# Kernel optimization log

Measured on AMD Instinct MI355X. Metric: run time of the kernel, lower is better.

## Reference

```python
import jax, jax.numpy as jnp
import numpy as np

DIM = 384
DIM_HEAD = 32
HEADS = DIM // DIM_HEAD  # 12
WIN = 8
DIM_FF = 1536
FUSED = DIM + DIM + DIM_FF  # 2304


def setup_inputs() -> dict:
    key = jax.random.key(0)
    ks = jax.random.split(key, 8)
    B, H, W = 16, 64, 64
    x = jax.random.normal(ks[0], (B, DIM, H, W), dtype=jnp.float32)
    s = lambda fan_in: 1.0 / np.sqrt(fan_in)
    w_fused = jax.random.normal(ks[1], (FUSED, DIM), dtype=jnp.float32) * s(DIM)
    w_gate = jax.random.normal(ks[2], (HEADS, DIM), dtype=jnp.float32) * s(DIM)
    b_gate = jnp.full((HEADS,), 0.5, dtype=jnp.float32)  # init_constant_(0.5)
    w_attn_out = jax.random.normal(ks[3], (DIM, DIM), dtype=jnp.float32) * s(DIM)
    w_ff_out = jax.random.normal(ks[4], (DIM, DIM_FF), dtype=jnp.float32) * s(DIM_FF)
    # StarReLU learnable scalars (metaformer defaults)
    sr_scale = jnp.asarray(0.8944, dtype=jnp.float32)
    sr_bias = jnp.asarray(-0.4472, dtype=jnp.float32)
    return {"x": x, "w_fused": w_fused, "w_gate": w_gate, "b_gate": b_gate,
            "w_attn_out": w_attn_out, "w_ff_out": w_ff_out,
            "sr_scale": sr_scale, "sr_bias": sr_bias}


def reference(x, w_fused, w_gate, b_gate, w_attn_out, w_ff_out, sr_scale, sr_bias):
    B, C, H, W = x.shape
    p = WIN
    gh, gw = H // p, W // p
    n = p * p
    # b c (h p1) (w p2) -> (b h w) (p1 p2) c
    xw = x.reshape(B, C, gh, p, gw, p).transpose(0, 2, 4, 3, 5, 1).reshape(B * gh * gw, n, C)
    fused = jnp.einsum('bnc,fc->bnf', xw, w_fused)  # [Bw, n, 2304]
    q, kv, x_ff = jnp.split(fused, [DIM, 2 * DIM], axis=-1)
    # b n (h d) -> b h n d
    q = q.reshape(-1, n, HEADS, DIM_HEAD).transpose(0, 2, 1, 3)
    kv = kv.reshape(-1, n, HEADS, DIM_HEAD).transpose(0, 2, 1, 3)
    scale = 1.0 / np.sqrt(DIM_HEAD)
    scores = jnp.einsum('bhnd,bhmd->bhnm', q, kv) * scale
    attn = jax.nn.softmax(scores, axis=-1)
    x_attn = jnp.einsum('bhnm,bhmd->bhnd', attn, kv)  # kv is both key and value
    gate = jnp.einsum('bnc,hc->bnh', xw, w_gate) + b_gate  # [Bw, n, heads]
    x_attn = x_attn * jax.nn.sigmoid(gate.transpose(0, 2, 1)[..., None])
    x_attn = x_attn.transpose(0, 2, 1, 3).reshape(-1, n, DIM)
    ff = sr_scale * jnp.square(jax.nn.relu(x_ff)) + sr_bias  # StarReLU
    out = jnp.einsum('bnc,oc->bno', x_attn, w_attn_out) + jnp.einsum('bnf,of->bno', ff, w_ff_out)
    # (b h w) (p1 p2) c -> b c (h p1) (w p2)
    out = out.reshape(B, gh, gw, p, p, C).transpose(0, 5, 1, 3, 2, 4).reshape(B, C, H, W)
    return out
```

## Files before the change

### kernel.cpp

```cpp
#include <hip/hip_runtime.h>
#include <hip/hip_bf16.h>

typedef __bf16 bf16x8 __attribute__((ext_vector_type(8), may_alias));
typedef float f32x4 __attribute__((ext_vector_type(4), may_alias));
typedef unsigned short ushort_a __attribute__((may_alias));

#define MFMA(a, b, c) __builtin_amdgcn_mfma_f32_16x16x32_bf16(a, b, c, 0, 0, 0)

__device__ __forceinline__ unsigned short f2bf(float f) {
  return __builtin_bit_cast(unsigned short, (__bf16)f);
}


__global__ __launch_bounds__(256) void prep_weights(
    const float* __restrict__ wf, const float* __restrict__ wg,
    const float* __restrict__ wao, const float* __restrict__ wfo,
    unsigned short* __restrict__ ws) {
  int i = blockIdx.x * 256 + threadIdx.x;
  if (i < 884736) { ws[i] = f2bf(wf[i]); return; }
  int j = i - 884736;
  if (j < 6144) { ws[i] = f2bf(j < 4608 ? wg[j] : 0.0f); return; }
  j -= 6144;
  if (j < 147456) { ws[i] = f2bf(wao[j]); return; }
  j -= 147456;
  if (j < 589824) ws[i] = f2bf(wfo[j]);
}


__global__ __launch_bounds__(512, 2) void fused_main(
    const float* __restrict__ x,
    const float* __restrict__ bgate,
    const float* __restrict__ srs,
    const float* __restrict__ srb,
    const unsigned short* __restrict__ wsb,
    float* __restrict__ out) {
  const unsigned short* wfB  = wsb;
  const unsigned short* wgB  = wsb + 884736;
  const unsigned short* waoB = wsb + 890880;
  const unsigned short* wfoB = wsb + 1038336;

  __shared__ __align__(16) char smem[114688];
  char* As  = smem;
  char* Stg = smem + 98304;

  const int tid = threadIdx.x;
  const int lane = tid & 63, wave = tid >> 6;
  const int l15 = lane & 15, l4 = lane >> 4;
  const int pair = wave >> 1, nb = (wave & 1) * 32;
  char* PB  = smem + 49152 + pair * 12288;
  char* KTb = PB + 8192;

  const int g  = blockIdx.x;
  const int wi = (g & 7) * 128 + (g >> 3);
  const int b = wi >> 6, ghi = (wi >> 3) & 7, gwi = wi & 7;
  const int h0 = ghi * 8, w0 = gwi * 8;

  {
    const float* xb = x + (size_t)b * 1572864 + h0 * 64 + w0;
    for (int it = 0; it < 6; ++it) {
      int idx = it * 512 + tid;
      int c = idx % 384, p1 = idx / 384;
      const float* src = xb + (size_t)c * 4096 + p1 * 64;
      float4 v0 = *(const float4*)src;
      float4 v1 = *(const float4*)(src + 4);
      float f[8] = {v0.x, v0.y, v0.z, v0.w, v1.x, v1.y, v1.z, v1.w};
#pragma unroll
      for (int jj = 0; jj < 8; ++jj) {
        int row = p1 * 8 + jj;
        int byte = (row * 768 + c * 2) ^ ((row & 7) << 4);
        *(ushort_a*)(As + byte) = f2bf(f[jj]);
      }
    }
  }
  const float ss = srs[0], sbi = srb[0];
  __syncthreads();

  auto ldA = [&](int row, int ks) -> bf16x8 {
    int byte = (row * 768 + ks * 64 + l4 * 16) ^ ((row & 7) << 4);
    return *(const bf16x8*)(As + byte);
  };

  f32x4 gfr[2] = {};
  {
    const unsigned short* wg0 = wgB + (size_t)l15 * 384 + l4 * 8;
#pragma unroll 2
    for (int ks = 0; ks < 12; ++ks) {
      bf16x8 bg = *(const bf16x8*)(wg0 + ks * 32);
      bf16x8 a0 = ldA(nb + l15, ks), a1 = ldA(nb + 16 + l15, ks);
      gfr[0] = MFMA(a0, bg, gfr[0]);
      gfr[1] = MFMA(a1, bg, gfr[1]);
    }
    float gb = (l15 < 12) ? bgate[l15] : 0.0f;
    gfr[0] += gb;
    gfr[1] += gb;
  }

  f32x4 of[4][3] = {};

#pragma unroll 1
  for (int r = 0; r < 3; ++r) {
    const int h = r * 4 + pair;
    f32x4 qf[2][2] = {}, kf[2][2] = {};
    const unsigned short* wq = wfB + ((size_t)(h * 32) + l15) * 384 + l4 * 8;
    const unsigned short* wk = wq + (size_t)384 * 384;
#pragma unroll 2
    for (int ks = 0; ks < 12; ++ks) {
      bf16x8 a0 = ldA(nb + l15, ks), a1 = ldA(nb + 16 + l15, ks);
#pragma unroll
      for (int nt = 0; nt < 2; ++nt) {
        bf16x8 bq = *(const bf16x8*)(wq + (size_t)nt * 16 * 384 + ks * 32);
        bf16x8 bk = *(const bf16x8*)(wk + (size_t)nt * 16 * 384 + ks * 32);
        qf[0][nt] = MFMA(a0, bq, qf[0][nt]);
        qf[1][nt] = MFMA(a1, bq, qf[1][nt]);
        kf[0][nt] = MFMA(a0, bk, kf[0][nt]);
        kf[1][nt] = MFMA(a1, bk, kf[1][nt]);
      }
    }
#pragma unroll
    for (int mt = 0; mt < 2; ++mt)
#pragma unroll
      for (int nt = 0; nt < 2; ++nt)
#pragma unroll
        for (int rr = 0; rr < 4; ++rr) {
          int n = nb + mt * 16 + l4 * 4 + rr;
          int d = nt * 16 + l15;
          int sw = (n & 7) << 4;
          *(ushort_a*)(PB + ((n * 128 + d * 2) ^ sw)) =
              f2bf(qf[mt][nt][rr] * 0.176776695f);
          unsigned short kvv = f2bf(kf[mt][nt][rr]);
          *(ushort_a*)(PB + ((n * 128 + 64 + d * 2) ^ sw)) = kvv;
          *(ushort_a*)(KTb + ((d * 128 + n * 2) ^ ((d & 7) << 4))) = kvv;
        }
    __syncthreads();
    f32x4 sf[2][4] = {};
    {
      bf16x8 bkv[4];
#pragma unroll
      for (int ni = 0; ni < 4; ++ni) {
        int m = ni * 16 + l15;
        bkv[ni] = *(const bf16x8*)(PB + ((m * 128 + 64 + l4 * 16) ^ ((m & 7) << 4)));
      }
#pragma unroll
      for (int mt = 0; mt < 2; ++mt) {
        int n = nb + mt * 16 + l15;
        bf16x8 aq = *(const bf16x8*)(PB + ((n * 128 + l4 * 16) ^ ((n & 7) << 4)));
#pragma unroll
        for (int ni = 0; ni < 4; ++ni) sf[mt][ni] = MFMA(aq, bkv[ni], sf[mt][ni]);
      }
    }
    __syncthreads();
#pragma unroll
    for (int mt = 0; mt < 2; ++mt) {
#pragma unroll
      for (int rr = 0; rr < 4; ++rr) {
        float v0 = sf[mt][0][rr], v1 = sf[mt][1][rr],
              v2 = sf[mt][2][rr], v3 = sf[mt][3][rr];
        float mx = fmaxf(fmaxf(v0, v1), fmaxf(v2, v3));
        mx = fmaxf(mx, __shfl_xor(mx, 1, 64));
        mx = fmaxf(mx, __shfl_xor(mx, 2, 64));
        mx = fmaxf(mx, __shfl_xor(mx, 4, 64));
        mx = fmaxf(mx, __shfl_xor(mx, 8, 64));
        float e0 = __expf(v0 - mx), e1 = __expf(v1 - mx),
              e2 = __expf(v2 - mx), e3 = __expf(v3 - mx);
        float sm = e0 + e1 + e2 + e3;
        sm += __shfl_xor(sm, 1, 64);
        sm += __shfl_xor(sm, 2, 64);
        sm += __shfl_xor(sm, 4, 64);
        sm += __shfl_xor(sm, 8, 64);
        float rs = 1.0f / sm;
        int n = nb + mt * 16 + l4 * 4 + rr;
        int base = n * 128, sw = (n & 7) << 4;
        *(ushort_a*)(PB + ((base + l15 * 2) ^ sw))      = f2bf(e0 * rs);
        *(ushort_a*)(PB + ((base + 32 + l15 * 2) ^ sw)) = f2bf(e1 * rs);
        *(ushort_a*)(PB + ((base + 64 + l15 * 2) ^ sw)) = f2bf(e2 * rs);
        *(ushort_a*)(PB + ((base + 96 + l15 * 2) ^ sw)) = f2bf(e3 * rs);
      }
    }
    f32x4 xo[2][2] = {};
#pragma unroll
    for (int ks = 0; ks < 2; ++ks) {
      bf16x8 bv[2];
#pragma unroll
      for (int nt = 0; nt < 2; ++nt) {
        int d = nt * 16 + l15;
        bv[nt] = *(const bf16x8*)(KTb + ((d * 128 + ks * 64 + l4 * 16) ^ ((d & 7) << 4)));
      }
#pragma unroll
      for (int mt = 0; mt < 2; ++mt) {
        int n = nb + mt * 16 + l15;
        bf16x8 ap = *(const bf16x8*)(PB + ((n * 128 + ks * 64 + l4 * 16) ^ ((n & 7) << 4)));
        xo[mt][0] = MFMA(ap, bv[0], xo[mt][0]);
        xo[mt][1] = MFMA(ap, bv[1], xo[mt][1]);
      }
    }
#pragma unroll
    for (int mt = 0; mt < 2; ++mt) {
#pragma unroll
      for (int rr = 0; rr < 4; ++rr) {
        float gv = __shfl(gfr[mt][rr], (lane & 48) | h, 64);
        float sg = 1.0f / (1.0f + __expf(-gv));
        int n = nb + mt * 16 + l4 * 4 + rr;
        int sw = (n & 7) << 4;
        int c0 = pair * 32 + l15;
        *(ushort_a*)(Stg + ((n * 256 + c0 * 2) ^ sw))        = f2bf(xo[mt][0][rr] * sg);
        *(ushort_a*)(Stg + ((n * 256 + (c0 + 16) * 2) ^ sw)) = f2bf(xo[mt][1][rr] * sg);
      }
    }
    __syncthreads();
    {
      const unsigned short* wao0 =
          waoB + (size_t)(wave * 48 + l15) * 384 + r * 128 + l4 * 8;
#pragma unroll
      for (int ks = 0; ks < 4; ++ks) {
        int kb = ks * 64 + l4 * 16, sz = (l15 & 7) << 4;
        bf16x8 a0 = *(const bf16x8*)(Stg + ((l15 * 256 + kb) ^ sz));
        bf16x8 a1 = *(const bf16x8*)(Stg + (((16 + l15) * 256 + kb) ^ sz));
        bf16x8 a2 = *(const bf16x8*)(Stg + (((32 + l15) * 256 + kb) ^ sz));
        bf16x8 a3 = *(const bf16x8*)(Stg + (((48 + l15) * 256 + kb) ^ sz));
#pragma unroll
        for (int nt = 0; nt < 3; ++nt) {
          bf16x8 bw = *(const bf16x8*)(wao0 + (size_t)nt * 16 * 384 + ks * 32);
          of[0][nt] = MFMA(a0, bw, of[0][nt]);
          of[1][nt] = MFMA(a1, bw, of[1][nt]);
          of[2][nt] = MFMA(a2, bw, of[2][nt]);
          of[3][nt] = MFMA(a3, bw, of[3][nt]);
        }
      }
    }
  }

#pragma unroll 1
  for (int tg = 0; tg < 6; ++tg) {
    f32x4 ffr[4][2] = {};
    const unsigned short* wfin0 =
        wfB + (size_t)(768 + tg * 256 + wave * 16 + l15) * 384 + l4 * 8;
    const unsigned short* wfin1 = wfin0 + (size_t)128 * 384;
#pragma unroll 2
    for (int ks = 0; ks < 12; ++ks) {
      bf16x8 a0 = ldA(l15, ks), a1 = ldA(16 + l15, ks),
             a2 = ldA(32 + l15, ks), a3 = ldA(48 + l15, ks);
      bf16x8 bw0 = *(const bf16x8*)(wfin0 + ks * 32);
      ffr[0][0] = MFMA(a0, bw0, ffr[0][0]);
      ffr[1][0] = MFMA(a1, bw0, ffr[1][0]);
      ffr[2][0] = MFMA(a2, bw0, ffr[2][0]);
      ffr[3][0] = MFMA(a3, bw0, ffr[3][0]);
      bf16x8 bw1 = *(const bf16x8*)(wfin1 + ks * 32);
      ffr[0][1] = MFMA(a0, bw1, ffr[0][1]);
      ffr[1][1] = MFMA(a1, bw1, ffr[1][1]);
      ffr[2][1] = MFMA(a2, bw1, ffr[2][1]);
      ffr[3][1] = MFMA(a3, bw1, ffr[3][1]);
    }
#pragma unroll
    for (int u = 0; u < 2; ++u) {
      char* fb = smem + 49152 + u * 16384;
#pragma unroll
      for (int mt = 0; mt < 4; ++mt)
#pragma unroll
        for (int rr = 0; rr < 4; ++rr) {
          float v = fmaxf(ffr[mt][u][rr], 0.0f);
          v = ss * v * v + sbi;
          int n = mt * 16 + l4 * 4 + rr;
          int cw = wave * 16 + l15;
          *(ushort_a*)(fb + ((n * 256 + cw * 2) ^ ((n & 7) << 4))) = f2bf(v);
        }
    }
    __syncthreads();
#pragma unroll 1
    for (int u = 0; u < 2; ++u) {
      char* fb = smem + 49152 + u * 16384;
      const unsigned short* wfo2 =
          wfoB + (size_t)(wave * 48 + l15) * 1536 + (tg * 2 + u) * 128 + l4 * 8;
#pragma unroll
      for (int ks = 0; ks < 4; ++ks) {
        int kb = ks * 64 + l4 * 16, sz = (l15 & 7) << 4;
        bf16x8 a0 = *(const bf16x8*)(fb + ((l15 * 256 + kb) ^ sz));
        bf16x8 a1 = *(const bf16x8*)(fb + (((16 + l15) * 256 + kb) ^ sz));
        bf16x8 a2 = *(const bf16x8*)(fb + (((32 + l15) * 256 + kb) ^ sz));
        bf16x8 a3 = *(const bf16x8*)(fb + (((48 + l15) * 256 + kb) ^ sz));
#pragma unroll
        for (int nt = 0; nt < 3; ++nt) {
          bf16x8 bw = *(const bf16x8*)(wfo2 + (size_t)nt * 16 * 1536 + ks * 32);
          of[0][nt] = MFMA(a0, bw, of[0][nt]);
          of[1][nt] = MFMA(a1, bw, of[1][nt]);
          of[2][nt] = MFMA(a2, bw, of[2][nt]);
          of[3][nt] = MFMA(a3, bw, of[3][nt]);
        }
      }
    }
    __syncthreads();
  }

  float* ob = out + (size_t)b * 1572864 + h0 * 64 + w0;
#pragma unroll
  for (int nt = 0; nt < 3; ++nt) {
    int col = wave * 48 + nt * 16 + l15;
    float* oc = ob + (size_t)col * 4096;
#pragma unroll
    for (int mt = 0; mt < 4; ++mt) {
      int n0 = mt * 16 + l4 * 4;
      *(f32x4*)(oc + (n0 >> 3) * 64 + (n0 & 7)) = of[mt][nt];
    }
  }
}

extern "C" void kernel_launch(void* const* d_in, const int* in_sizes, int n_in,
                              void* d_out, int out_size, void* d_ws, size_t ws_size,
                              hipStream_t stream) {
  const float* x   = (const float*)d_in[0];
  const float* wf  = (const float*)d_in[1];
  const float* wg  = (const float*)d_in[2];
  const float* bg  = (const float*)d_in[3];
  const float* wao = (const float*)d_in[4];
  const float* wfo = (const float*)d_in[5];
  const float* srs = (const float*)d_in[6];
  const float* srb = (const float*)d_in[7];
  unsigned short* ws = (unsigned short*)d_ws;

  prep_weights<<<6360, 256, 0, stream>>>(wf, wg, wao, wfo, ws);
  fused_main<<<1024, 512, 0, stream>>>(x, bg, srs, srb, ws, (float*)d_out);
}
```

Before: 573.4 us.

## Split fused window kernel into gather, tiled GEMM, attention, and output GEMM stages

Replaces the single per-window fused kernel with four kernels: a gather that transposes x into bf16 token-major rows, a 128x128 tiled double-buffered GEMM producing q/kv/StarReLU-ff and gate activations into workspace, a per-window attention kernel, and a tiled output GEMM over concatenated attention and ff features. The aim is better weight reuse and MFMA tiling than the per-window kernel, which re-streamed all weights per 64-token window. In exchange it adds large intermediate bf16 tensors in global memory (~700MB workspace) and extra launches. It falls back to the old fused kernel if the workspace is too small.

```diff
diff --git a/kernel.cpp b/kernel.cpp
--- a/kernel.cpp
+++ b/kernel.cpp
@@ -4,13 +4,26 @@
 typedef __bf16 bf16x8 __attribute__((ext_vector_type(8), may_alias));
 typedef float f32x4 __attribute__((ext_vector_type(4), may_alias));
 typedef unsigned short ushort_a __attribute__((may_alias));
+typedef unsigned int uint_a __attribute__((may_alias));
+typedef unsigned short us8 __attribute__((ext_vector_type(8), may_alias));
 
 #define MFMA(a, b, c) __builtin_amdgcn_mfma_f32_16x16x32_bf16(a, b, c, 0, 0, 0)
 
 __device__ __forceinline__ unsigned short f2bf(float f) {
   return __builtin_bit_cast(unsigned short, (__bf16)f);
 }
-
+__device__ __forceinline__ float bf2f(unsigned short u) {
+  unsigned v = ((unsigned)u) << 16;
+  return __builtin_bit_cast(float, v);
+}
+
+#define OFF_WG 884736
+#define OFF_WAO 933888
+#define OFF_WFO 1081344
+#define OFF_XG 1671168
+#define OFF_FUSED 26836992
+#define OFF_GATE 177831936
+#define WS_NEED 357761024ull
 
 __global__ __launch_bounds__(256) void prep_weights(
     const float* __restrict__ wf, const float* __restrict__ wg,
@@ -19,42 +32,360 @@
   int i = blockIdx.x * 256 + threadIdx.x;
   if (i < 884736) { ws[i] = f2bf(wf[i]); return; }
   int j = i - 884736;
-  if (j < 6144) { ws[i] = f2bf(j < 4608 ? wg[j] : 0.0f); return; }
-  j -= 6144;
+  if (j < 49152) { ws[i] = f2bf(j < 4608 ? wg[j] : 0.0f); return; }
+  j -= 49152;
   if (j < 147456) { ws[i] = f2bf(wao[j]); return; }
   j -= 147456;
   if (j < 589824) ws[i] = f2bf(wfo[j]);
 }
 
-
-__global__ __launch_bounds__(512, 2) void fused_main(
-    const float* __restrict__ x,
-    const float* __restrict__ bgate,
-    const float* __restrict__ srs,
-    const float* __restrict__ srb,
-    const unsigned short* __restrict__ wsb,
-    float* __restrict__ out) {
-  const unsigned short* wfB  = wsb;
-  const unsigned short* wgB  = wsb + 884736;
-  const unsigned short* waoB = wsb + 890880;
-  const unsigned short* wfoB = wsb + 1038336;
-
+__global__ __launch_bounds__(256) void k0_gather(const float* __restrict__ x,
+                                                 unsigned short* __restrict__ xg) {
+  __shared__ __align__(16) char As[49152];
+  int tid = threadIdx.x, wi = blockIdx.x;
+  int b = wi >> 6, ghi = (wi >> 3) & 7, gwi = wi & 7;
+  const float* xb = x + (size_t)b * 1572864 + (ghi * 8) * 64 + gwi * 8;
+  for (int it = 0; it < 12; ++it) {
+    int idx = it * 256 + tid;
+    int c = idx % 384, p1 = idx / 384;
+    const float* src = xb + (size_t)c * 4096 + p1 * 64;
+    float4 v0 = *(const float4*)src, v1 = *(const float4*)(src + 4);
+    float f[8] = {v0.x, v0.y, v0.z, v0.w, v1.x, v1.y, v1.z, v1.w};
+#pragma unroll
+    for (int jj = 0; jj < 8; ++jj) {
+      int row = p1 * 8 + jj;
+      int byte = (row * 768 + c * 2) ^ ((row & 7) << 4);
+      *(ushort_a*)(As + byte) = f2bf(f[jj]);
+    }
+  }
+  __syncthreads();
+  unsigned short* og = xg + (size_t)wi * 24576;
+#pragma unroll
+  for (int it = 0; it < 12; ++it) {
+    int idx = it * 256 + tid;
+    int row = idx / 48, c = idx % 48;
+    int byte = (row * 768 + c * 16) ^ ((row & 7) << 4);
+    *(us8*)(og + (size_t)row * 384 + c * 8) = *(us8*)(As + byte);
+  }
+}
+
+__global__ __launch_bounds__(512, 4) void k1_gemm(unsigned short* __restrict__ ws,
+                                                  const float* __restrict__ srs,
+                                                  const float* __restrict__ srb) {
+  __shared__ __align__(16) char sm[65536];
+  const int tid = threadIdx.x, lane = tid & 63, wave = tid >> 6;
+  const int l15 = lane & 15, l4 = lane >> 4;
+  const int wr = wave & 3, wc = wave >> 2;
+  const int bid = blockIdx.x, mb = bid & 511, nb = bid >> 9;
+  const unsigned short* Ab = ws + OFF_XG + (size_t)mb * 128 * 384;
+  const unsigned short* Bb =
+      (nb < 18) ? ws + (size_t)nb * 128 * 384 : ws + OFF_WG;
+  const int srow = tid >> 3, sc = tid & 7;
+  f32x4 of[2][4] = {};
+  us8 stA[2], stB[2];
+#pragma unroll
+  for (int r2 = 0; r2 < 2; ++r2) {
+    int row = srow + 64 * r2;
+    stA[r2] = *(const us8*)(Ab + (size_t)row * 384 + sc * 8);
+    stB[r2] = *(const us8*)(Bb + (size_t)row * 384 + sc * 8);
+  }
+#pragma unroll
+  for (int r2 = 0; r2 < 2; ++r2) {
+    int row = srow + 64 * r2;
+    int byte = (row * 128 + sc * 16) ^ ((row & 7) << 4);
+    *(us8*)(sm + byte) = stA[r2];
+    *(us8*)(sm + 32768 + byte) = stB[r2];
+  }
+  __syncthreads();
+#pragma unroll 1
+  for (int ks = 0; ks < 6; ++ks) {
+    int cur = (ks & 1) * 16384;
+    if (ks < 5) {
+#pragma unroll
+      for (int r2 = 0; r2 < 2; ++r2) {
+        int row = srow + 64 * r2;
+        stA[r2] = *(const us8*)(Ab + (size_t)row * 384 + (ks + 1) * 64 + sc * 8);
+        stB[r2] = *(const us8*)(Bb + (size_t)row * 384 + (ks + 1) * 64 + sc * 8);
+      }
+    }
+#pragma unroll
+    for (int kk = 0; kk < 2; ++kk) {
+      bf16x8 af[2], bfr[4];
+#pragma unroll
+      for (int mt = 0; mt < 2; ++mt) {
+        int row = wr * 32 + mt * 16 + l15;
+        af[mt] = *(const bf16x8*)(sm + cur +
+                                  ((row * 128 + kk * 64 + l4 * 16) ^ ((row & 7) << 4)));
+      }
+#pragma unroll
+      for (int nt = 0; nt < 4; ++nt) {
+        int row = wc * 64 + nt * 16 + l15;
+        bfr[nt] = *(const bf16x8*)(sm + 32768 + cur +
+                                   ((row * 128 + kk * 64 + l4 * 16) ^ ((row & 7) << 4)));
+      }
+#pragma unroll
+      for (int mt = 0; mt < 2; ++mt)
+#pragma unroll
+        for (int nt = 0; nt < 4; ++nt)
+          of[mt][nt] = MFMA(af[mt], bfr[nt], of[mt][nt]);
+    }
+    if (ks < 5) {
+      int nxt = ((ks + 1) & 1) * 16384;
+#pragma unroll
+      for (int r2 = 0; r2 < 2; ++r2) {
+        int row = srow + 64 * r2;
+        int byte = (row * 128 + sc * 16) ^ ((row & 7) << 4);
+        *(us8*)(sm + nxt + byte) = stA[r2];
+        *(us8*)(sm + 32768 + nxt + byte) = stB[r2];
+      }
+    }
+    __syncthreads();
+  }
+  const float ssc = srs[0], sbi = srb[0];
+  const bool ffreg = (nb >= 6) && (nb < 18);
+#pragma unroll
+  for (int mt = 0; mt < 2; ++mt)
+#pragma unroll
+    for (int nt = 0; nt < 4; ++nt)
+#pragma unroll
+      for (int rr = 0; rr < 4; ++rr) {
+        int row = wr * 32 + mt * 16 + l4 * 4 + rr;
+        int col = wc * 64 + nt * 16 + l15;
+        float v = of[mt][nt][rr];
+        if (ffreg) { v = fmaxf(v, 0.0f); v = ssc * v * v + sbi; }
+        *(ushort_a*)(sm + ((row * 256 + col * 2) ^ ((row & 7) << 4))) = f2bf(v);
+      }
+  __syncthreads();
+  if (nb < 18) {
+    unsigned short* fo = ws + OFF_FUSED + (size_t)mb * 128 * 2304 + nb * 128;
+#pragma unroll
+    for (int r2 = 0; r2 < 4; ++r2) {
+      int idx = r2 * 512 + tid;
+      int row = idx >> 4, c = idx & 15;
+      int byte = (row * 256 + c * 16) ^ ((row & 7) << 4);
+      *(us8*)(fo + (size_t)row * 2304 + c * 8) = *(us8*)(sm + byte);
+    }
+  } else {
+    unsigned short* go = ws + OFF_GATE + (size_t)mb * 128 * 16;
+#pragma unroll
+    for (int r2 = 0; r2 < 4; ++r2) {
+      int idx = r2 * 512 + tid;
+      int row = idx >> 4, c = idx & 15;
+      if (c < 2) {
+        int byte = (row * 256 + c * 16) ^ ((row & 7) << 4);
+        *(us8*)(go + (size_t)row * 16 + c * 8) = *(us8*)(sm + byte);
+      }
+    }
+  }
+}
+
+__global__ __launch_bounds__(256, 3) void k2_attn(unsigned short* __restrict__ ws,
+                                                  const float* __restrict__ bgate) {
+  __shared__ __align__(16) char sm[49152];
+  const int tid = threadIdx.x, lane = tid & 63, wave = tid >> 6;
+  const int l15 = lane & 15, l4 = lane >> 4;
+  char* kvT = sm + wave * 12288;
+  char* Pb = kvT + 4096;
+  const int wi = blockIdx.x;
+  const size_t T0 = (size_t)wi * 64;
+  unsigned short* fused = ws + OFF_FUSED;
+  const unsigned short* gb = ws + OFF_GATE;
+  const f32x4 zz = {};
+#pragma unroll 1
+  for (int hi = 0; hi < 3; ++hi) {
+    const int h = wave + hi * 4;
+    bf16x8 akv[4], bq[4];
+#pragma unroll
+    for (int t = 0; t < 4; ++t) {
+      akv[t] = *(const bf16x8*)(fused + (T0 + t * 16 + l15) * 2304 + 384 + h * 32 + l4 * 8);
+      bq[t] = *(const bf16x8*)(fused + (T0 + t * 16 + l15) * 2304 + h * 32 + l4 * 8);
+    }
+    f32x4 sfT[4][4];
+#pragma unroll
+    for (int mt = 0; mt < 4; ++mt)
+#pragma unroll
+      for (int ni = 0; ni < 4; ++ni) sfT[mt][ni] = MFMA(akv[mt], bq[ni], zz);
+#pragma unroll
+    for (int mt = 0; mt < 4; ++mt) {
+      us8 u = __builtin_bit_cast(us8, akv[mt]);
+      int m = mt * 16 + l15;
+#pragma unroll
+      for (int j = 0; j < 8; ++j) {
+        int d = l4 * 8 + j;
+        *(ushort_a*)(kvT + ((d * 128 + m * 2) ^ ((d & 7) << 4))) = u[j];
+      }
+    }
+#pragma unroll
+    for (int ni = 0; ni < 4; ++ni) {
+      float s[16];
+#pragma unroll
+      for (int mt = 0; mt < 4; ++mt)
+#pragma unroll
+        for (int rr = 0; rr < 4; ++rr)
+          s[mt * 4 + rr] = sfT[mt][ni][rr] * 0.176776695f;
+      float mx = s[0];
+#pragma unroll
+      for (int q2 = 1; q2 < 16; ++q2) mx = fmaxf(mx, s[q2]);
+      mx = fmaxf(mx, __shfl_xor(mx, 16, 64));
+      mx = fmaxf(mx, __shfl_xor(mx, 32, 64));
+      float sum = 0.0f;
+#pragma unroll
+      for (int q2 = 0; q2 < 16; ++q2) {
+        s[q2] = __expf(s[q2] - mx);
+        sum += s[q2];
+      }
+      sum += __shfl_xor(sum, 16, 64);
+      sum += __shfl_xor(sum, 32, 64);
+      float rs = 1.0f / sum;
+      int n = ni * 16 + l15;
+      int rowb = n * 128, sw = (n & 7) << 4;
+#pragma unroll
+      for (int mt = 0; mt < 4; ++mt) {
+        int m = mt * 16 + l4 * 4;
+        unsigned p0 = (unsigned)f2bf(s[mt * 4 + 0] * rs) |
+                      ((unsigned)f2bf(s[mt * 4 + 1] * rs) << 16);
+        unsigned p1 = (unsigned)f2bf(s[mt * 4 + 2] * rs) |
+                      ((unsigned)f2bf(s[mt * 4 + 3] * rs) << 16);
+        *(uint_a*)(Pb + ((rowb + m * 2) ^ sw)) = p0;
+        *(uint_a*)(Pb + ((rowb + (m + 2) * 2) ^ sw)) = p1;
+      }
+    }
+    f32x4 xo[4][2] = {};
+#pragma unroll
+    for (int ks = 0; ks < 2; ++ks) {
+      bf16x8 bv[2];
+#pragma unroll
+      for (int dt = 0; dt < 2; ++dt) {
+        int d = dt * 16 + l15;
+        bv[dt] = *(const bf16x8*)(kvT + ((d * 128 + ks * 64 + l4 * 16) ^ ((d & 7) << 4)));
+      }
+#pragma unroll
+      for (int nt = 0; nt < 4; ++nt) {
+        int n = nt * 16 + l15;
+        bf16x8 ap = *(const bf16x8*)(Pb + ((n * 128 + ks * 64 + l4 * 16) ^ ((n & 7) << 4)));
+        xo[nt][0] = MFMA(ap, bv[0], xo[nt][0]);
+        xo[nt][1] = MFMA(ap, bv[1], xo[nt][1]);
+      }
+    }
+    const float bgh = bgate[h];
+#pragma unroll
+    for (int nt = 0; nt < 4; ++nt)
+#pragma unroll
+      for (int rr = 0; rr < 4; ++rr) {
+        int n = nt * 16 + l4 * 4 + rr;
+        float gv = bf2f(gb[(T0 + n) * 16 + h]) + bgh;
+        float sg = 1.0f / (1.0f + __expf(-gv));
+#pragma unroll
+        for (int dt = 0; dt < 2; ++dt)
+          fused[(T0 + n) * 2304 + h * 32 + dt * 16 + l15] =
+              f2bf(xo[nt][dt][rr] * sg);
+      }
+  }
+}
+
+__global__ __launch_bounds__(512, 4) void k3_gemm(const unsigned short* __restrict__ ws,
+                                                  float* __restrict__ out) {
+  __shared__ __align__(16) char sm[65536];
+  const int tid = threadIdx.x, lane = tid & 63, wave = tid >> 6;
+  const int l15 = lane & 15, l4 = lane >> 4;
+  const int wr = wave & 3, wc = wave >> 2;
+  const int bid = blockIdx.x, mb = bid & 511, nB = bid >> 9;
+  const size_t T0 = (size_t)mb * 128;
+  const unsigned short* fA = ws + OFF_FUSED + T0 * 2304;
+  const unsigned short* wao = ws + OFF_WAO + (size_t)(nB * 128) * 384;
+  const unsigned short* wfo = ws + OFF_WFO + (size_t)(nB * 128) * 1536;
+  const int srow = tid >> 3, sc = tid & 7;
+  f32x4 of[2][4] = {};
+  us8 stA[2], stB[2];
+  auto loadAB = [&](int ks) {
+    int ac = ks < 6 ? ks * 64 : 768 + (ks - 6) * 64;
+#pragma unroll
+    for (int r2 = 0; r2 < 2; ++r2) {
+      int row = srow + 64 * r2;
+      stA[r2] = *(const us8*)(fA + (size_t)row * 2304 + ac + sc * 8);
+      if (ks < 6)
+        stB[r2] = *(const us8*)(wao + (size_t)row * 384 + ks * 64 + sc * 8);
+      else
+        stB[r2] = *(const us8*)(wfo + (size_t)row * 1536 + (ks - 6) * 64 + sc * 8);
+    }
+  };
+  auto writeAB = [&](int buf) {
+#pragma unroll
+    for (int r2 = 0; r2 < 2; ++r2) {
+      int row = srow + 64 * r2;
+      int byte = (row * 128 + sc * 16) ^ ((row & 7) << 4);
+      *(us8*)(sm + buf + byte) = stA[r2];
+      *(us8*)(sm + 32768 + buf + byte) = stB[r2];
+    }
+  };
+  loadAB(0);
+  writeAB(0);
+  __syncthreads();
+#pragma unroll 1
+  for (int ks = 0; ks < 30; ++ks) {
+    int cur = (ks & 1) * 16384;
+    if (ks < 29) loadAB(ks + 1);
+#pragma unroll
+    for (int kk = 0; kk < 2; ++kk) {
+      bf16x8 af[2], bfr[4];
+#pragma unroll
+      for (int mt = 0; mt < 2; ++mt) {
+        int row = wr * 32 + mt * 16 + l15;
+        af[mt] = *(const bf16x8*)(sm + cur +
+                                  ((row * 128 + kk * 64 + l4 * 16) ^ ((row & 7) << 4)));
+      }
+#pragma unroll
+      for (int nt = 0; nt < 4; ++nt) {
+        int row = wc * 64 + nt * 16 + l15;
+        bfr[nt] = *(const bf16x8*)(sm + 32768 + cur +
+                                   ((row * 128 + kk * 64 + l4 * 16) ^ ((row & 7) << 4)));
+      }
+#pragma unroll
+      for (int mt = 0; mt < 2; ++mt)
+#pragma unroll
+        for (int nt = 0; nt < 4; ++nt)
+          of[mt][nt] = MFMA(af[mt], bfr[nt], of[mt][nt]);
+    }
+    if (ks < 29) writeAB(((ks + 1) & 1) * 16384);
+    __syncthreads();
+  }
+#pragma unroll
+  for (int mt = 0; mt < 2; ++mt) {
+    int n0 = wr * 32 + mt * 16 + l4 * 4;
+    int T = (int)T0 + n0;
+    int wi = T >> 6, n = T & 63;
+    int b = wi >> 6, ghi = (wi >> 3) & 7, gwi = wi & 7;
+    float* ob = out + (size_t)b * 1572864 + (size_t)(ghi * 8 + (n >> 3)) * 64 +
+                gwi * 8 + (n & 7);
+#pragma unroll
+    for (int nt = 0; nt < 4; ++nt) {
+      int c = nB * 128 + wc * 64 + nt * 16 + l15;
+      *(f32x4*)(ob + (size_t)c * 4096) = of[mt][nt];
+    }
+  }
+}
+
+__global__ __launch_bounds__(512, 2) void fused_fallback(
+    const float* __restrict__ x, const float* __restrict__ bgate,
+    const float* __restrict__ srs, const float* __restrict__ srb,
+    const unsigned short* __restrict__ wsb, float* __restrict__ out) {
+  const unsigned short* wfB = wsb;
+  const unsigned short* wgB = wsb + OFF_WG;
+  const unsigned short* waoB = wsb + OFF_WAO;
+  const unsigned short* wfoB = wsb + OFF_WFO;
   __shared__ __align__(16) char smem[114688];
-  char* As  = smem;
+  char* As = smem;
   char* Stg = smem + 98304;
-
   const int tid = threadIdx.x;
   const int lane = tid & 63, wave = tid >> 6;
   const int l15 = lane & 15, l4 = lane >> 4;
   const int pair = wave >> 1, nb = (wave & 1) * 32;
-  char* PB  = smem + 49152 + pair * 12288;
+  char* PB = smem + 49152 + pair * 12288;
   char* KTb = PB + 8192;
-
-  const int g  = blockIdx.x;
+  const int g = blockIdx.x;
   const int wi = (g & 7) * 128 + (g >> 3);
   const int b = wi >> 6, ghi = (wi >> 3) & 7, gwi = wi & 7;
   const int h0 = ghi * 8, w0 = gwi * 8;
-
   {
     const float* xb = x + (size_t)b * 1572864 + h0 * 64 + w0;
     for (int it = 0; it < 6; ++it) {
@@ -74,12 +405,10 @@
   }
   const float ss = srs[0], sbi = srb[0];
   __syncthreads();
-
   auto ldA = [&](int row, int ks) -> bf16x8 {
     int byte = (row * 768 + ks * 64 + l4 * 16) ^ ((row & 7) << 4);
     return *(const bf16x8*)(As + byte);
   };
-
   f32x4 gfr[2] = {};
   {
     const unsigned short* wg0 = wgB + (size_t)l15 * 384 + l4 * 8;
@@ -94,9 +423,7 @@
     gfr[0] += gb;
     gfr[1] += gb;
   }
-
   f32x4 of[4][3] = {};
-
 #pragma unroll 1
   for (int r = 0; r < 3; ++r) {
     const int h = r * 4 + pair;
@@ -153,24 +480,24 @@
     for (int mt = 0; mt < 2; ++mt) {
 #pragma unroll
       for (int rr = 0; rr < 4; ++rr) {
-        float v0 = sf[mt][0][rr], v1 = sf[mt][1][rr],
-              v2 = sf[mt][2][rr], v3 = sf[mt][3][rr];
+        float v0 = sf[mt][0][rr], v1 = sf[mt][1][rr], v2 = sf[mt][2][rr],
+              v3 = sf[mt][3][rr];
         float mx = fmaxf(fmaxf(v0, v1), fmaxf(v2, v3));
         mx = fmaxf(mx, __shfl_xor(mx, 1, 64));
         mx = fmaxf(mx, __shfl_xor(mx, 2, 64));
         mx = fmaxf(mx, __shfl_xor(mx, 4, 64));
         mx = fmaxf(mx, __shfl_xor(mx, 8, 64));
-        float e0 = __expf(v0 - mx), e1 = __expf(v1 - mx),
-              e2 = __expf(v2 - mx), e3 = __expf(v3 - mx);
-        float sm = e0 + e1 + e2 + e3;
-        sm += __shfl_xor(sm, 1, 64);
-        sm += __shfl_xor(sm, 2, 64);
-        sm += __shfl_xor(sm, 4, 64);
-        sm += __shfl_xor(sm, 8, 64);
-        float rs = 1.0f / sm;
+        float e0 = __expf(v0 - mx), e1 = __expf(v1 - mx), e2 = __expf(v2 - mx),
+              e3 = __expf(v3 - mx);
+        float sm2 = e0 + e1 + e2 + e3;
+        sm2 += __shfl_xor(sm2, 1, 64);
+        sm2 += __shfl_xor(sm2, 2, 64);
+        sm2 += __shfl_xor(sm2, 4, 64);
+        sm2 += __shfl_xor(sm2, 8, 64);
+        float rs = 1.0f / sm2;
         int n = nb + mt * 16 + l4 * 4 + rr;
         int base = n * 128, sw = (n & 7) << 4;
-        *(ushort_a*)(PB + ((base + l15 * 2) ^ sw))      = f2bf(e0 * rs);
+        *(ushort_a*)(PB + ((base + l15 * 2) ^ sw)) = f2bf(e0 * rs);
         *(ushort_a*)(PB + ((base + 32 + l15 * 2) ^ sw)) = f2bf(e1 * rs);
         *(ushort_a*)(PB + ((base + 64 + l15 * 2) ^ sw)) = f2bf(e2 * rs);
         *(ushort_a*)(PB + ((base + 96 + l15 * 2) ^ sw)) = f2bf(e3 * rs);
@@ -202,7 +529,7 @@
         int n = nb + mt * 16 + l4 * 4 + rr;
         int sw = (n & 7) << 4;
         int c0 = pair * 32 + l15;
-        *(ushort_a*)(Stg + ((n * 256 + c0 * 2) ^ sw))        = f2bf(xo[mt][0][rr] * sg);
+        *(ushort_a*)(Stg + ((n * 256 + c0 * 2) ^ sw)) = f2bf(xo[mt][0][rr] * sg);
         *(ushort_a*)(Stg + ((n * 256 + (c0 + 16) * 2) ^ sw)) = f2bf(xo[mt][1][rr] * sg);
       }
     }
@@ -228,7 +555,6 @@
       }
     }
   }
-
 #pragma unroll 1
   for (int tg = 0; tg < 6; ++tg) {
     f32x4 ffr[4][2] = {};
@@ -237,8 +563,8 @@
     const unsigned short* wfin1 = wfin0 + (size_t)128 * 384;
 #pragma unroll 2
     for (int ks = 0; ks < 12; ++ks) {
-      bf16x8 a0 = ldA(l15, ks), a1 = ldA(16 + l15, ks),
-             a2 = ldA(32 + l15, ks), a3 = ldA(48 + l15, ks);
+      bf16x8 a0 = ldA(l15, ks), a1 = ldA(16 + l15, ks), a2 = ldA(32 + l15, ks),
+             a3 = ldA(48 + l15, ks);
       bf16x8 bw0 = *(const bf16x8*)(wfin0 + ks * 32);
       ffr[0][0] = MFMA(a0, bw0, ffr[0][0]);
       ffr[1][0] = MFMA(a1, bw0, ffr[1][0]);
@@ -289,7 +615,6 @@
     }
     __syncthreads();
   }
-
   float* ob = out + (size_t)b * 1572864 + h0 * 64 + w0;
 #pragma unroll
   for (int nt = 0; nt < 3; ++nt) {
@@ -306,16 +631,23 @@
 extern "C" void kernel_launch(void* const* d_in, const int* in_sizes, int n_in,
                               void* d_out, int out_size, void* d_ws, size_t ws_size,
                               hipStream_t stream) {
-  const float* x   = (const float*)d_in[0];
-  const float* wf  = (const float*)d_in[1];
-  const float* wg  = (const float*)d_in[2];
-  const float* bg  = (const float*)d_in[3];
+  const float* x = (const float*)d_in[0];
+  const float* wf = (const float*)d_in[1];
+  const float* wg = (const float*)d_in[2];
+  const float* bg = (const float*)d_in[3];
   const float* wao = (const float*)d_in[4];
   const float* wfo = (const float*)d_in[5];
   const float* srs = (const float*)d_in[6];
   const float* srb = (const float*)d_in[7];
   unsigned short* ws = (unsigned short*)d_ws;
 
-  prep_weights<<<6360, 256, 0, stream>>>(wf, wg, wao, wfo, ws);
-  fused_main<<<1024, 512, 0, stream>>>(x, bg, srs, srb, ws, (float*)d_out);
-}
+  prep_weights<<<6528, 256, 0, stream>>>(wf, wg, wao, wfo, ws);
+  if (ws_size >= WS_NEED) {
+    k0_gather<<<1024, 256, 0, stream>>>(x, ws + OFF_XG);
+    k1_gemm<<<512 * 19, 512, 0, stream>>>(ws, srs, srb);
+    k2_attn<<<1024, 256, 0, stream>>>(ws, bg);
+    k3_gemm<<<512 * 3, 512, 0, stream>>>(ws, (float*)d_out);
+  } else {
+    fused_fallback<<<1024, 512, 0, stream>>>(x, bg, srs, srb, ws, (float*)d_out);
+  }
+}
```

New measurement: 537.1 us. 1.07x faster.
